# Kernel optimization log

Measured on AMD Instinct MI355X. Metric: run time of the kernel, lower is better.

Reference implementation:

```python
import jax, jax.numpy as jnp
import numpy as np


def setup_inputs() -> dict:
    key = jax.random.key(0)
    ks = jax.random.split(key, 7)
    B, S, D, H, Dh = 4, 2048, 1024, 16, 64
    return {
        "query_input": jax.random.normal(ks[0], (B, S, D), jnp.float32),
        "key_input": jax.random.normal(ks[1], (B, S, D), jnp.float32),
        "value_input": jax.random.normal(ks[2], (B, S, D), jnp.float32),
        "Wq": jax.random.normal(ks[3], (D, H, Dh), jnp.float32) * 0.03,
        "Wk": jax.random.normal(ks[4], (D, H, Dh), jnp.float32) * 0.03,
        "Wv": jax.random.normal(ks[5], (D, H, Dh), jnp.float32) * 0.03,
        "Wo": jax.random.normal(ks[6], (H, Dh, D), jnp.float32) * 0.03,
    }


def reference(query_input, key_input, value_input, Wq, Wk, Wv, Wo):
    # Projections: [B,S,D] x [D,H,Dh] -> [B,S,H,Dh]
    q = jnp.einsum("bsd,dhk->bshk", query_input, Wq)
    k = jnp.einsum("bsd,dhk->bshk", key_input, Wk)
    v = jnp.einsum("bsd,dhk->bshk", value_input, Wv)
    depth = Wq.shape[-1]
    q = q * (depth ** -0.5)
    # logits: [B,H,F,T]  (F = query len, T = key len)
    logits = jnp.einsum("bthk,bfhk->bhft", k, q)
    weights = jax.nn.softmax(logits, axis=-1)
    # attention output: [B,F,H,Dh]
    ctx = jnp.einsum("bhft,bthk->bfhk", weights, v)
    # output projection: [B,F,H,Dh] x [H,Dh,D] -> [B,F,D]
    return jnp.einsum("bfhk,hkd->bfd", ctx, Wo)
```

## Files before the change

### kernel.cpp

```cpp
#include <hip/hip_runtime.h>
#include <stdint.h>

typedef __bf16 bf16;
typedef __bf16 bf16x4 __attribute__((ext_vector_type(4)));
typedef __bf16 bf16x8 __attribute__((ext_vector_type(8)));
typedef float f32x4 __attribute__((ext_vector_type(4)));

#define AS1 __attribute__((address_space(1)))
#define AS3 __attribute__((address_space(3)))

__device__ __forceinline__ void async16(void* lds, const void* g) {
    __builtin_amdgcn_global_load_lds((AS1 void*)g, (AS3 void*)lds, 16, 0, 0);
}

__global__ __launch_bounds__(256) void cvt_bf16_3(const float* __restrict__ x0,
                                                  const float* __restrict__ x1,
                                                  const float* __restrict__ x2,
                                                  bf16* __restrict__ y0,
                                                  bf16* __restrict__ y1,
                                                  bf16* __restrict__ y2, int n) {
    const int z = blockIdx.z;
    const float* x = z == 0 ? x0 : z == 1 ? x1 : x2;
    bf16* y = z == 0 ? y0 : z == 1 ? y1 : y2;
    int i = (blockIdx.x * 256 + threadIdx.x) * 8;
    if (i + 8 <= n) {
        f32x4 a = *(const f32x4*)(x + i);
        f32x4 b = *(const f32x4*)(x + i + 4);
        bf16x8 o;
#pragma unroll
        for (int j = 0; j < 4; ++j) { o[j] = (bf16)a[j]; o[4 + j] = (bf16)b[j]; }
        *(bf16x8*)(y + i) = o;
    }
}

__global__ __launch_bounds__(256) void transpose_cvt4(
    const float* __restrict__ s0, const float* __restrict__ s1,
    const float* __restrict__ s2, const float* __restrict__ s3,
    bf16* __restrict__ d0, bf16* __restrict__ d1,
    bf16* __restrict__ d2, bf16* __restrict__ d3) {
    const int z = blockIdx.z;
    const float* W = z == 0 ? s0 : z == 1 ? s1 : z == 2 ? s2 : s3;
    bf16* Wt = z == 0 ? d0 : z == 1 ? d1 : z == 2 ? d2 : d3;
    const int K = 1024, N = 1024;
    __shared__ float Ts[64 * 65];
    const int t = threadIdx.x;
    const int c = t & 63, r0 = t >> 6;
    const int k0 = blockIdx.x * 64, n0 = blockIdx.y * 64;
#pragma unroll
    for (int i = 0; i < 16; ++i) {
        int r = r0 + i * 4;
        Ts[r * 65 + c] = W[(size_t)(k0 + r) * N + n0 + c];
    }
    __syncthreads();
#pragma unroll
    for (int i = 0; i < 16; ++i) {
        int r = r0 + i * 4;
        Wt[(size_t)(n0 + r) * K + k0 + c] = (bf16)Ts[c * 65 + r];
    }
}

template <typename OutT>
__device__ __forceinline__ void gemm_body(const bf16* __restrict__ A,
                                          const bf16* __restrict__ Bt,
                                          OutT* __restrict__ C,
                                          int N, int K, float scale,
                                          int m0, int n0,
                                          bf16* As, bf16* Bs) {
    const int t = threadIdx.x;
    const int lane = t & 63;
    const int w = t >> 6;
    const int l15 = lane & 15;
    const int quad = lane >> 4;
    const int wm = w >> 1, wn = w & 1;

    f32x4 acc[4][4];
#pragma unroll
    for (int i = 0; i < 4; ++i)
#pragma unroll
        for (int j = 0; j < 4; ++j) acc[i][j] = (f32x4){0.f, 0.f, 0.f, 0.f};

    const int c0 = t, c1 = t + 256;
    const bf16* gA0 = A + (size_t)(m0 + (c0 >> 2)) * K + (c0 & 3) * 8;
    const bf16* gA1 = A + (size_t)(m0 + (c1 >> 2)) * K + (c1 & 3) * 8;
    const bf16* gB0 = Bt + (size_t)(n0 + (c0 >> 2)) * K + (c0 & 3) * 8;
    const bf16* gB1 = Bt + (size_t)(n0 + (c1 >> 2)) * K + (c1 & 3) * 8;
    bf16* lA0 = As + w * 512;
    bf16* lA1 = As + 2048 + w * 512;
    bf16* lB0 = Bs + w * 512;
    bf16* lB1 = Bs + 2048 + w * 512;

    for (int k0 = 0; k0 < K; k0 += 32) {
        __syncthreads();
        async16(lA0, gA0 + k0);
        async16(lA1, gA1 + k0);
        async16(lB0, gB0 + k0);
        async16(lB1, gB1 + k0);
        __syncthreads();
        bf16x8 af[4], bfv[4];
#pragma unroll
        for (int mi = 0; mi < 4; ++mi)
            af[mi] = *(const bf16x8*)&As[(wm * 64 + mi * 16 + l15) * 32 + quad * 8];
#pragma unroll
        for (int ni = 0; ni < 4; ++ni)
            bfv[ni] = *(const bf16x8*)&Bs[(wn * 64 + ni * 16 + l15) * 32 + quad * 8];
#pragma unroll
        for (int mi = 0; mi < 4; ++mi)
#pragma unroll
            for (int ni = 0; ni < 4; ++ni)
                acc[mi][ni] = __builtin_amdgcn_mfma_f32_16x16x32_bf16(
                    af[mi], bfv[ni], acc[mi][ni], 0, 0, 0);
    }

#pragma unroll
    for (int mi = 0; mi < 4; ++mi)
#pragma unroll
        for (int ni = 0; ni < 4; ++ni)
#pragma unroll
            for (int r = 0; r < 4; ++r) {
                int row = m0 + wm * 64 + mi * 16 + quad * 4 + r;
                int col = n0 + wn * 64 + ni * 16 + l15;
                C[(size_t)row * N + col] = (OutT)(acc[mi][ni][r] * scale);
            }
}

__global__ __launch_bounds__(256) void gemm_qkv(
    const bf16* __restrict__ Xq, const bf16* __restrict__ Xk, const bf16* __restrict__ Xv,
    const bf16* __restrict__ Wqt, const bf16* __restrict__ Wkt, const bf16* __restrict__ Wvt,
    bf16* __restrict__ Qb, bf16* __restrict__ Kb, bf16* __restrict__ VtG) {
    __shared__ __align__(16) bf16 As[128 * 32];
    __shared__ __align__(16) bf16 Bs[128 * 32];
    const int z = blockIdx.z;
    const int blk = blockIdx.x;
    const bf16* A; const bf16* Bt; bf16* C; int N; float scale; int m0, n0;
    if (z == 0) { A = Xq; Bt = Wqt; C = Qb; N = 1024; scale = 0.125f;
                  m0 = (blk >> 3) * 128; n0 = (blk & 7) * 128; }
    else if (z == 1) { A = Xk; Bt = Wkt; C = Kb; N = 1024; scale = 1.0f;
                  m0 = (blk >> 3) * 128; n0 = (blk & 7) * 128; }
    else { A = Wvt; Bt = Xv; C = VtG; N = 8192; scale = 1.0f;
                  m0 = (blk >> 6) * 128; n0 = (blk & 63) * 128; }
    gemm_body<bf16>(A, Bt, C, N, 1024, scale, m0, n0, As, Bs);
}

__global__ __launch_bounds__(256) void gemm_out(const bf16* __restrict__ A,
                                                const bf16* __restrict__ Bt,
                                                float* __restrict__ C) {
    __shared__ __align__(16) bf16 As[128 * 32];
    __shared__ __align__(16) bf16 Bs[128 * 32];
    gemm_body<float>(A, Bt, C, 1024, 1024, 1.0f, blockIdx.y * 128, blockIdx.x * 128,
                     As, Bs);
}

__global__ __launch_bounds__(256) void attn_fa(const bf16* __restrict__ Q,
                                               const bf16* __restrict__ K,
                                               const bf16* __restrict__ Vt,
                                               bf16* __restrict__ O) {
    __shared__ __align__(16) bf16 Ks[64 * 64];
    __shared__ __align__(16) bf16 Vs[64 * 64];
    __shared__ __align__(16) bf16 Pt[4][32 * 72];

    const int t = threadIdx.x;
    const int lane = t & 63;
    const int w = t >> 6;
    const int l15 = lane & 15;
    const int quad = lane >> 4;
    const int bh = blockIdx.y;
    const int b = bh >> 4, h = bh & 15;
    const int q0 = blockIdx.x * 128;
    const size_t baseQ = (size_t)b * 2048 * 1024 + (size_t)h * 64;
    const float L2E = 1.44269504088896340736f;

    const int r0s = t >> 3,          g0s = (t & 7) ^ (r0s & 7);
    const int r1s = (t + 256) >> 3,  g1s = ((t + 256) & 7) ^ (r1s & 7);
    const bf16* gK0 = K + baseQ + (size_t)r0s * 1024 + g0s * 8;
    const bf16* gK1 = K + baseQ + (size_t)r1s * 1024 + g1s * 8;
    const bf16* gV0 = Vt + (size_t)(h * 64 + r0s) * 8192 + (size_t)b * 2048 + g0s * 8;
    const bf16* gV1 = Vt + (size_t)(h * 64 + r1s) * 8192 + (size_t)b * 2048 + g1s * 8;
    bf16* lc0 = (bf16*)Ks + w * 512;
    bf16* lc1 = (bf16*)Ks + 2048 + w * 512;

    bf16x8 qf[2][2];
#pragma unroll
    for (int mi = 0; mi < 2; ++mi)
#pragma unroll
        for (int kk = 0; kk < 2; ++kk)
            qf[mi][kk] = *(const bf16x8*)(Q + baseQ +
                (size_t)(q0 + w * 32 + mi * 16 + l15) * 1024 + kk * 32 + quad * 8);

    f32x4 accO[4][2];
    float l_part[2] = {0.f, 0.f};
#pragma unroll
    for (int nd = 0; nd < 4; ++nd)
#pragma unroll
        for (int mi = 0; mi < 2; ++mi) accO[nd][mi] = (f32x4){0.f, 0.f, 0.f, 0.f};

    auto swz = [&](int r, int g) { return (r * 8 + (g ^ (r & 7))) * 8; };

    for (int t0 = 0; t0 < 2048; t0 += 64) {
        __syncthreads();
        async16(lc0, gK0 + (size_t)t0 * 1024);
        async16(lc1, gK1 + (size_t)t0 * 1024);
        async16((bf16*)Vs + w * 512, gV0 + t0);
        async16((bf16*)Vs + 2048 + w * 512, gV1 + t0);
        __syncthreads();

        f32x4 accS[4][2];
#pragma unroll
        for (int nt = 0; nt < 4; ++nt)
#pragma unroll
            for (int mi = 0; mi < 2; ++mi) accS[nt][mi] = (f32x4){0.f, 0.f, 0.f, 0.f};
#pragma unroll
        for (int kk = 0; kk < 2; ++kk) {
            bf16x8 kf[4];
#pragma unroll
            for (int nt = 0; nt < 4; ++nt)
                kf[nt] = *(const bf16x8*)&Ks[swz(nt * 16 + l15, kk * 4 + quad)];
#pragma unroll
            for (int nt = 0; nt < 4; ++nt)
#pragma unroll
                for (int mi = 0; mi < 2; ++mi)
                    accS[nt][mi] = __builtin_amdgcn_mfma_f32_16x16x32_bf16(
                        kf[nt], qf[mi][kk], accS[nt][mi], 0, 0, 0);
        }

        bf16* Pp = &Pt[w][0];
#pragma unroll
        for (int mi = 0; mi < 2; ++mi) {
            float rs = 0.f;
#pragma unroll
            for (int nt = 0; nt < 4; ++nt) {
                bf16x4 pk;
#pragma unroll
                for (int r = 0; r < 4; ++r) {
                    float p = __builtin_amdgcn_exp2f(accS[nt][mi][r] * L2E);
                    rs += p;
                    pk[r] = (bf16)p;
                }
                *(bf16x4*)&Pp[(mi * 16 + l15) * 72 + nt * 16 + quad * 4] = pk;
            }
            l_part[mi] += rs;
        }

#pragma unroll
        for (int kk = 0; kk < 2; ++kk) {
            bf16x8 vf[4], pf[2];
#pragma unroll
            for (int nd = 0; nd < 4; ++nd)
                vf[nd] = *(const bf16x8*)&Vs[swz(nd * 16 + l15, kk * 4 + quad)];
#pragma unroll
            for (int mi = 0; mi < 2; ++mi)
                pf[mi] = *(const bf16x8*)&Pp[(mi * 16 + l15) * 72 + kk * 32 + quad * 8];
#pragma unroll
            for (int nd = 0; nd < 4; ++nd)
#pragma unroll
                for (int mi = 0; mi < 2; ++mi)
                    accO[nd][mi] = __builtin_amdgcn_mfma_f32_16x16x32_bf16(
                        vf[nd], pf[mi], accO[nd][mi], 0, 0, 0);
        }
    }

    float inv[2];
#pragma unroll
    for (int mi = 0; mi < 2; ++mi) {
        float l = l_part[mi];
        l += __shfl_xor(l, 16);
        l += __shfl_xor(l, 32);
        inv[mi] = 1.0f / l;
    }

#pragma unroll
    for (int mi = 0; mi < 2; ++mi) {
        size_t rowoff = baseQ + (size_t)(q0 + w * 32 + mi * 16 + l15) * 1024;
#pragma unroll
        for (int nd = 0; nd < 4; ++nd) {
            bf16x4 o;
#pragma unroll
            for (int r = 0; r < 4; ++r) o[r] = (bf16)(accO[nd][mi][r] * inv[mi]);
            *(bf16x4*)&O[rowoff + nd * 16 + quad * 4] = o;
        }
    }
}

extern "C" void kernel_launch(void* const* d_in, const int* in_sizes, int n_in,
                              void* d_out, int out_size, void* d_ws, size_t ws_size,
                              hipStream_t stream) {
    const float* qin = (const float*)d_in[0];
    const float* kin = (const float*)d_in[1];
    const float* vin = (const float*)d_in[2];
    const float* Wq = (const float*)d_in[3];
    const float* Wk = (const float*)d_in[4];
    const float* Wv = (const float*)d_in[5];
    const float* Wo = (const float*)d_in[6];
    float* out = (float*)d_out;

    const int M = 8192, D = 1024;
    char* ws = (char*)d_ws;
    bf16* Xq  = (bf16*)(ws);
    bf16* Xk  = (bf16*)(ws + ((size_t)16 << 20));
    bf16* Xv  = (bf16*)(ws + ((size_t)32 << 20));
    bf16* Qb  = (bf16*)(ws + ((size_t)48 << 20));
    bf16* Kb  = (bf16*)(ws + ((size_t)64 << 20));
    bf16* VtG = (bf16*)(ws + ((size_t)80 << 20));
    bf16* Cb  = (bf16*)(ws);
    bf16* Wqt = (bf16*)(ws + ((size_t)96 << 20));
    bf16* Wkt = Wqt + 1024 * 1024;
    bf16* Wvt = Wkt + 1024 * 1024;
    bf16* Wot = Wvt + 1024 * 1024;

    transpose_cvt4<<<dim3(16, 16, 4), 256, 0, stream>>>(Wq, Wk, Wv, Wo,
                                                        Wqt, Wkt, Wvt, Wot);
    cvt_bf16_3<<<dim3(4096, 1, 3), 256, 0, stream>>>(qin, kin, vin, Xq, Xk, Xv, M * D);
    gemm_qkv<<<dim3(512, 1, 3), 256, 0, stream>>>(Xq, Xk, Xv, Wqt, Wkt, Wvt,
                                                  Qb, Kb, VtG);
    attn_fa<<<dim3(16, 64), 256, 0, stream>>>(Qb, Kb, VtG, Cb);
    gemm_out<<<dim3(8, 64), 256, 0, stream>>>(Cb, Wot, out);
}
```

Measured before the change: 345.9 us.

## Double-buffer attention K/V tiles, widen GEMM K-tile with swizzle, merge prep kernels

The attention kernel now double-buffers its K and V LDS tiles, so the async loads for the next key block are issued while the current one is computed, and one barrier per iteration is dropped. The GEMM body moves from a 32-wide to a 64-wide K tile, which halves the barrier count, and applies an XOR swizzle to the LDS layout to avoid bank conflicts. The input conversion and weight transpose kernels are merged into one launch. In exchange LDS use rises, which may reduce occupancy, and many blocks in the fourth z slice of the merged kernel exit immediately.

```diff
diff --git a/kernel.cpp b/kernel.cpp
--- a/kernel.cpp
+++ b/kernel.cpp
@@ -13,49 +13,46 @@
     __builtin_amdgcn_global_load_lds((AS1 void*)g, (AS3 void*)lds, 16, 0, 0);
 }
 
-__global__ __launch_bounds__(256) void cvt_bf16_3(const float* __restrict__ x0,
-                                                  const float* __restrict__ x1,
-                                                  const float* __restrict__ x2,
-                                                  bf16* __restrict__ y0,
-                                                  bf16* __restrict__ y1,
-                                                  bf16* __restrict__ y2, int n) {
-    const int z = blockIdx.z;
-    const float* x = z == 0 ? x0 : z == 1 ? x1 : x2;
-    bf16* y = z == 0 ? y0 : z == 1 ? y1 : y2;
-    int i = (blockIdx.x * 256 + threadIdx.x) * 8;
-    if (i + 8 <= n) {
-        f32x4 a = *(const f32x4*)(x + i);
-        f32x4 b = *(const f32x4*)(x + i + 4);
-        bf16x8 o;
-#pragma unroll
-        for (int j = 0; j < 4; ++j) { o[j] = (bf16)a[j]; o[4 + j] = (bf16)b[j]; }
-        *(bf16x8*)(y + i) = o;
-    }
-}
-
-__global__ __launch_bounds__(256) void transpose_cvt4(
+__global__ __launch_bounds__(256) void prep(
+    const float* __restrict__ x0, const float* __restrict__ x1,
+    const float* __restrict__ x2,
+    bf16* __restrict__ y0, bf16* __restrict__ y1, bf16* __restrict__ y2,
     const float* __restrict__ s0, const float* __restrict__ s1,
     const float* __restrict__ s2, const float* __restrict__ s3,
     bf16* __restrict__ d0, bf16* __restrict__ d1,
     bf16* __restrict__ d2, bf16* __restrict__ d3) {
     const int z = blockIdx.z;
-    const float* W = z == 0 ? s0 : z == 1 ? s1 : z == 2 ? s2 : s3;
-    bf16* Wt = z == 0 ? d0 : z == 1 ? d1 : z == 2 ? d2 : d3;
-    const int K = 1024, N = 1024;
+    const int t = threadIdx.x;
+    if (z < 3) {
+        const float* x = z == 0 ? x0 : z == 1 ? x1 : x2;
+        bf16* y = z == 0 ? y0 : z == 1 ? y1 : y2;
+        int i = (blockIdx.x * 256 + t) * 8;
+        f32x4 a = *(const f32x4*)(x + i);
+        f32x4 b = *(const f32x4*)(x + i + 4);
+        bf16x8 o;
+#pragma unroll
+        for (int j = 0; j < 4; ++j) { o[j] = (bf16)a[j]; o[4 + j] = (bf16)b[j]; }
+        *(bf16x8*)(y + i) = o;
+        return;
+    }
+    const int bx = blockIdx.x;
+    if (bx >= 1024) return;
+    const int wsel = bx >> 8, tile = bx & 255;
+    const float* W = wsel == 0 ? s0 : wsel == 1 ? s1 : wsel == 2 ? s2 : s3;
+    bf16* Wt = wsel == 0 ? d0 : wsel == 1 ? d1 : wsel == 2 ? d2 : d3;
+    const int k0 = (tile >> 4) * 64, n0 = (tile & 15) * 64;
     __shared__ float Ts[64 * 65];
-    const int t = threadIdx.x;
     const int c = t & 63, r0 = t >> 6;
-    const int k0 = blockIdx.x * 64, n0 = blockIdx.y * 64;
 #pragma unroll
     for (int i = 0; i < 16; ++i) {
         int r = r0 + i * 4;
-        Ts[r * 65 + c] = W[(size_t)(k0 + r) * N + n0 + c];
+        Ts[r * 65 + c] = W[(size_t)(k0 + r) * 1024 + n0 + c];
     }
     __syncthreads();
 #pragma unroll
     for (int i = 0; i < 16; ++i) {
         int r = r0 + i * 4;
-        Wt[(size_t)(n0 + r) * K + k0 + c] = (bf16)Ts[c * 65 + r];
+        Wt[(size_t)(n0 + r) * 1024 + k0 + c] = (bf16)Ts[c * 65 + r];
     }
 }
 
@@ -79,36 +76,44 @@
 #pragma unroll
         for (int j = 0; j < 4; ++j) acc[i][j] = (f32x4){0.f, 0.f, 0.f, 0.f};
 
-    const int c0 = t, c1 = t + 256;
-    const bf16* gA0 = A + (size_t)(m0 + (c0 >> 2)) * K + (c0 & 3) * 8;
-    const bf16* gA1 = A + (size_t)(m0 + (c1 >> 2)) * K + (c1 & 3) * 8;
-    const bf16* gB0 = Bt + (size_t)(n0 + (c0 >> 2)) * K + (c0 & 3) * 8;
-    const bf16* gB1 = Bt + (size_t)(n0 + (c1 >> 2)) * K + (c1 & 3) * 8;
-    bf16* lA0 = As + w * 512;
-    bf16* lA1 = As + 2048 + w * 512;
-    bf16* lB0 = Bs + w * 512;
-    bf16* lB1 = Bs + 2048 + w * 512;
-
-    for (int k0 = 0; k0 < K; k0 += 32) {
+    const bf16* gA[4];
+    const bf16* gB[4];
+#pragma unroll
+    for (int j = 0; j < 4; ++j) {
+        int c = j * 256 + t;
+        int row = c >> 3, g = (c & 7) ^ (row & 7);
+        gA[j] = A + (size_t)(m0 + row) * K + g * 8;
+        gB[j] = Bt + (size_t)(n0 + row) * K + g * 8;
+    }
+
+    for (int k0 = 0; k0 < K; k0 += 64) {
         __syncthreads();
-        async16(lA0, gA0 + k0);
-        async16(lA1, gA1 + k0);
-        async16(lB0, gB0 + k0);
-        async16(lB1, gB1 + k0);
+#pragma unroll
+        for (int j = 0; j < 4; ++j) {
+            async16(As + (j * 256 + w * 64) * 8, gA[j] + k0);
+            async16(Bs + (j * 256 + w * 64) * 8, gB[j] + k0);
+        }
         __syncthreads();
-        bf16x8 af[4], bfv[4];
-#pragma unroll
-        for (int mi = 0; mi < 4; ++mi)
-            af[mi] = *(const bf16x8*)&As[(wm * 64 + mi * 16 + l15) * 32 + quad * 8];
-#pragma unroll
-        for (int ni = 0; ni < 4; ++ni)
-            bfv[ni] = *(const bf16x8*)&Bs[(wn * 64 + ni * 16 + l15) * 32 + quad * 8];
-#pragma unroll
-        for (int mi = 0; mi < 4; ++mi)
-#pragma unroll
-            for (int ni = 0; ni < 4; ++ni)
-                acc[mi][ni] = __builtin_amdgcn_mfma_f32_16x16x32_bf16(
-                    af[mi], bfv[ni], acc[mi][ni], 0, 0, 0);
+#pragma unroll
+        for (int kk = 0; kk < 2; ++kk) {
+            bf16x8 af[4], bfv[4];
+#pragma unroll
+            for (int mi = 0; mi < 4; ++mi) {
+                int r = wm * 64 + mi * 16 + l15;
+                af[mi] = *(const bf16x8*)&As[r * 64 + (((kk * 4 + quad) ^ (r & 7)) * 8)];
+            }
+#pragma unroll
+            for (int ni = 0; ni < 4; ++ni) {
+                int r = wn * 64 + ni * 16 + l15;
+                bfv[ni] = *(const bf16x8*)&Bs[r * 64 + (((kk * 4 + quad) ^ (r & 7)) * 8)];
+            }
+#pragma unroll
+            for (int mi = 0; mi < 4; ++mi)
+#pragma unroll
+                for (int ni = 0; ni < 4; ++ni)
+                    acc[mi][ni] = __builtin_amdgcn_mfma_f32_16x16x32_bf16(
+                        af[mi], bfv[ni], acc[mi][ni], 0, 0, 0);
+        }
     }
 
 #pragma unroll
@@ -127,8 +132,8 @@
     const bf16* __restrict__ Xq, const bf16* __restrict__ Xk, const bf16* __restrict__ Xv,
     const bf16* __restrict__ Wqt, const bf16* __restrict__ Wkt, const bf16* __restrict__ Wvt,
     bf16* __restrict__ Qb, bf16* __restrict__ Kb, bf16* __restrict__ VtG) {
-    __shared__ __align__(16) bf16 As[128 * 32];
-    __shared__ __align__(16) bf16 Bs[128 * 32];
+    __shared__ __align__(16) bf16 As[128 * 64];
+    __shared__ __align__(16) bf16 Bs[128 * 64];
     const int z = blockIdx.z;
     const int blk = blockIdx.x;
     const bf16* A; const bf16* Bt; bf16* C; int N; float scale; int m0, n0;
@@ -144,8 +149,8 @@
 __global__ __launch_bounds__(256) void gemm_out(const bf16* __restrict__ A,
                                                 const bf16* __restrict__ Bt,
                                                 float* __restrict__ C) {
-    __shared__ __align__(16) bf16 As[128 * 32];
-    __shared__ __align__(16) bf16 Bs[128 * 32];
+    __shared__ __align__(16) bf16 As[128 * 64];
+    __shared__ __align__(16) bf16 Bs[128 * 64];
     gemm_body<float>(A, Bt, C, 1024, 1024, 1.0f, blockIdx.y * 128, blockIdx.x * 128,
                      As, Bs);
 }
@@ -154,8 +159,8 @@
                                                const bf16* __restrict__ K,
                                                const bf16* __restrict__ Vt,
                                                bf16* __restrict__ O) {
-    __shared__ __align__(16) bf16 Ks[64 * 64];
-    __shared__ __align__(16) bf16 Vs[64 * 64];
+    __shared__ __align__(16) bf16 Ks[2][64 * 64];
+    __shared__ __align__(16) bf16 Vs[2][64 * 64];
     __shared__ __align__(16) bf16 Pt[4][32 * 72];
 
     const int t = threadIdx.x;
@@ -175,8 +180,6 @@
     const bf16* gK1 = K + baseQ + (size_t)r1s * 1024 + g1s * 8;
     const bf16* gV0 = Vt + (size_t)(h * 64 + r0s) * 8192 + (size_t)b * 2048 + g0s * 8;
     const bf16* gV1 = Vt + (size_t)(h * 64 + r1s) * 8192 + (size_t)b * 2048 + g1s * 8;
-    bf16* lc0 = (bf16*)Ks + w * 512;
-    bf16* lc1 = (bf16*)Ks + 2048 + w * 512;
 
     bf16x8 qf[2][2];
 #pragma unroll
@@ -194,14 +197,20 @@
         for (int mi = 0; mi < 2; ++mi) accO[nd][mi] = (f32x4){0.f, 0.f, 0.f, 0.f};
 
     auto swz = [&](int r, int g) { return (r * 8 + (g ^ (r & 7))) * 8; };
-
-    for (int t0 = 0; t0 < 2048; t0 += 64) {
+    auto stage = [&](int t0, int bi) {
+        async16((bf16*)Ks[bi] + w * 512,        gK0 + (size_t)t0 * 1024);
+        async16((bf16*)Ks[bi] + 2048 + w * 512, gK1 + (size_t)t0 * 1024);
+        async16((bf16*)Vs[bi] + w * 512,        gV0 + t0);
+        async16((bf16*)Vs[bi] + 2048 + w * 512, gV1 + t0);
+    };
+
+    stage(0, 0);
+
+    for (int it = 0; it < 32; ++it) {
         __syncthreads();
-        async16(lc0, gK0 + (size_t)t0 * 1024);
-        async16(lc1, gK1 + (size_t)t0 * 1024);
-        async16((bf16*)Vs + w * 512, gV0 + t0);
-        async16((bf16*)Vs + 2048 + w * 512, gV1 + t0);
-        __syncthreads();
+        if (it + 1 < 32) stage((it + 1) * 64, (it + 1) & 1);
+        const bf16* Kb = Ks[it & 1];
+        const bf16* Vb = Vs[it & 1];
 
         f32x4 accS[4][2];
 #pragma unroll
@@ -213,7 +222,7 @@
             bf16x8 kf[4];
 #pragma unroll
             for (int nt = 0; nt < 4; ++nt)
-                kf[nt] = *(const bf16x8*)&Ks[swz(nt * 16 + l15, kk * 4 + quad)];
+                kf[nt] = *(const bf16x8*)&Kb[swz(nt * 16 + l15, kk * 4 + quad)];
 #pragma unroll
             for (int nt = 0; nt < 4; ++nt)
 #pragma unroll
@@ -245,7 +254,7 @@
             bf16x8 vf[4], pf[2];
 #pragma unroll
             for (int nd = 0; nd < 4; ++nd)
-                vf[nd] = *(const bf16x8*)&Vs[swz(nd * 16 + l15, kk * 4 + quad)];
+                vf[nd] = *(const bf16x8*)&Vb[swz(nd * 16 + l15, kk * 4 + quad)];
 #pragma unroll
             for (int mi = 0; mi < 2; ++mi)
                 pf[mi] = *(const bf16x8*)&Pp[(mi * 16 + l15) * 72 + kk * 32 + quad * 8];
@@ -292,7 +301,6 @@
     const float* Wo = (const float*)d_in[6];
     float* out = (float*)d_out;
 
-    const int M = 8192, D = 1024;
     char* ws = (char*)d_ws;
     bf16* Xq  = (bf16*)(ws);
     bf16* Xk  = (bf16*)(ws + ((size_t)16 << 20));
@@ -306,9 +314,8 @@
     bf16* Wvt = Wkt + 1024 * 1024;
     bf16* Wot = Wvt + 1024 * 1024;
 
-    transpose_cvt4<<<dim3(16, 16, 4), 256, 0, stream>>>(Wq, Wk, Wv, Wo,
-                                                        Wqt, Wkt, Wvt, Wot);
-    cvt_bf16_3<<<dim3(4096, 1, 3), 256, 0, stream>>>(qin, kin, vin, Xq, Xk, Xv, M * D);
+    prep<<<dim3(4096, 1, 4), 256, 0, stream>>>(qin, kin, vin, Xq, Xk, Xv,
+                                               Wq, Wk, Wv, Wo, Wqt, Wkt, Wvt, Wot);
     gemm_qkv<<<dim3(512, 1, 3), 256, 0, stream>>>(Xq, Xk, Xv, Wqt, Wkt, Wvt,
                                                   Qb, Kb, VtG);
     attn_fa<<<dim3(16, 64), 256, 0, stream>>>(Qb, Kb, VtG, Cb);
```

New measurement: 341.8 us. Within noise of the previous version (-1.2%).
